# Performance work log

Measured on AMD Instinct MI355X. Metric: run time of the kernel, lower is better.

Reference implementation:

```python
import jax, jax.numpy as jnp
import numpy as np
import math

B, N, D, H, K = 8, 256, 128, 256, 128


def setup_inputs() -> dict:
    key = jax.random.key(0)
    ks = jax.random.split(key, 8)
    # forward args
    x = jax.random.uniform(ks[0], (B, N, N), dtype=jnp.float32) * 3.0  # pairwise distances
    atom_embeds = jax.random.normal(ks[1], (B, N, D), dtype=jnp.float32)
    # params of nn.Linear(2D, H) and nn.Linear(H, 2) (store as [in, out])
    lim1 = 1.0 / math.sqrt(2 * D)
    W1 = jax.random.uniform(ks[2], (2 * D, H), minval=-lim1, maxval=lim1, dtype=jnp.float32)
    b1 = jax.random.uniform(ks[3], (H,), minval=-lim1, maxval=lim1, dtype=jnp.float32)
    lim2 = 1.0 / math.sqrt(H)
    W2 = jax.random.uniform(ks[4], (H, 2), minval=-lim2, maxval=lim2, dtype=jnp.float32)
    b2 = jax.random.uniform(ks[5], (2,), minval=-lim2, maxval=lim2, dtype=jnp.float32)
    # RBF params: means ~ U(0,3), temps ~ U(0.1,10)
    means = jax.random.uniform(ks[6], (K,), minval=0.0, maxval=3.0, dtype=jnp.float32)
    temps = jax.random.uniform(ks[7], (K,), minval=0.1, maxval=10.0, dtype=jnp.float32)
    return {"x": x, "atom_embeds": atom_embeds, "W1": W1, "b1": b1,
            "W2": W2, "b2": b2, "means": means, "temps": temps}


def reference(x, atom_embeds, W1, b1, W2, b2, means, temps):
    d = atom_embeds.shape[-1]
    scale = 1.0 / math.sqrt(2 * d)
    # Split-weight trick: cat([e_i, e_j]) @ W1 == e_i @ W1[:D] + e_j @ W1[D:]
    # (same math, avoids materializing the [B,N,N,2D] concat)
    hi = jnp.einsum('bnd,dh->bnh', atom_embeds, W1[:d])   # [B,N,H]
    hj = jnp.einsum('bnd,dh->bnh', atom_embeds, W1[d:])   # [B,N,H]
    h = jax.nn.relu(hi[:, :, None, :] + hj[:, None, :, :] + b1)  # [B,N,N,H]
    edge_features = (jnp.einsum('bijh,ho->bijo', h, W2) + b2) * scale  # [B,N,N,2]
    mul = edge_features[..., 0:1]   # [B,N,N,1]
    bias = edge_features[..., 1:2]  # [B,N,N,1]
    v = mul * x[..., None] + bias   # [B,N,N,1]
    temp = jnp.abs(temps)
    # RBF gaussian basis expansion -> [B,N,N,K]
    return jnp.exp(-jnp.square(v - means) * temp)
```

## Files before the change

kernel.cpp:

```cpp
#include <hip/hip_runtime.h>
#include <hip/hip_bf16.h>


#define NB 8
#define NN 256
#define ND 128
#define NH 256
#define NK 128

__global__ __launch_bounds__(256) void precompute_hij(
    const float* __restrict__ atom, const float* __restrict__ W1,
    const float* __restrict__ b1,
    float* __restrict__ hi, float* __restrict__ hjbT) {
  const int h = threadIdx.x;
  const int base = blockIdx.x * 8;
  const int b  = base >> 8;
  const int j0 = base & 255;
  __shared__ float a[8][ND];
  for (int t = threadIdx.x; t < 8 * ND; t += 256) {
    a[t >> 7][t & 127] = atom[(size_t)base * ND + t];
  }
  __syncthreads();
  float acc0[8], acc1[8];
  const float bv = b1[h];
#pragma unroll
  for (int r = 0; r < 8; ++r) { acc0[r] = 0.f; acc1[r] = bv; }
  for (int d = 0; d < ND; ++d) {
    const float w0 = W1[d * NH + h];
    const float w1 = W1[(ND + d) * NH + h];
#pragma unroll
    for (int r = 0; r < 8; ++r) {
      acc0[r] = fmaf(a[r][d], w0, acc0[r]);
      acc1[r] = fmaf(a[r][d], w1, acc1[r]);
    }
  }
#pragma unroll
  for (int r = 0; r < 8; ++r) {
    hi[(size_t)(base + r) * NH + h] = acc0[r];
    hjbT[((size_t)b * NH + h) * NN + (j0 + r)] = acc1[r];
  }
}

__global__ __launch_bounds__(256) void edge_rbf(
    const float* __restrict__ x,
    const float* __restrict__ hi, const float* __restrict__ hjbT,
    const float* __restrict__ W2, const float* __restrict__ b2,
    const float* __restrict__ means, const float* __restrict__ temps,
    float* __restrict__ out) {
  const int b    = blockIdx.x & 7;
  const int i    = blockIdx.x >> 3;
  const int bi   = b * NN + i;
  const int lane = threadIdx.x & 63;
  const int wave = threadIdx.x >> 6;

  __shared__ float part0[4][NN];
  __shared__ float part1[4][NN];
  __shared__ float vsh[NN];

  const float* __restrict__ hjrow = hjbT + ((size_t)b * NH + wave * 64) * NN;
  const float* __restrict__ hirow = hi + (size_t)bi * NH + wave * 64;
  const float* __restrict__ w2row = W2 + wave * 128;

  float acc0[4] = {0.f, 0.f, 0.f, 0.f};
  float acc1[4] = {0.f, 0.f, 0.f, 0.f};
#pragma unroll 8
  for (int hh = 0; hh < 64; ++hh) {
    const float4 hj4 = *reinterpret_cast<const float4*>(hjrow + (size_t)hh * NN + 4 * lane);
    const float hih = hirow[hh];
    const float w0  = w2row[2 * hh];
    const float w1  = w2row[2 * hh + 1];
    float a0 = fmaxf(hih + hj4.x, 0.f);
    float a1 = fmaxf(hih + hj4.y, 0.f);
    float a2 = fmaxf(hih + hj4.z, 0.f);
    float a3 = fmaxf(hih + hj4.w, 0.f);
    acc0[0] = fmaf(a0, w0, acc0[0]); acc1[0] = fmaf(a0, w1, acc1[0]);
    acc0[1] = fmaf(a1, w0, acc0[1]); acc1[1] = fmaf(a1, w1, acc1[1]);
    acc0[2] = fmaf(a2, w0, acc0[2]); acc1[2] = fmaf(a2, w1, acc1[2]);
    acc0[3] = fmaf(a3, w0, acc0[3]); acc1[3] = fmaf(a3, w1, acc1[3]);
  }
  *reinterpret_cast<float4*>(&part0[wave][4 * lane]) = make_float4(acc0[0], acc0[1], acc0[2], acc0[3]);
  *reinterpret_cast<float4*>(&part1[wave][4 * lane]) = make_float4(acc1[0], acc1[1], acc1[2], acc1[3]);
  __syncthreads();

  {
    const int t = threadIdx.x;
    const float s0 = part0[0][t] + part0[1][t] + part0[2][t] + part0[3][t];
    const float s1 = part1[0][t] + part1[1][t] + part1[2][t] + part1[3][t];
    const float scale = 0.0625f;
    const float mul  = (s0 + b2[0]) * scale;
    const float bias = (s1 + b2[1]) * scale;
    vsh[t] = fmaf(mul, x[(size_t)bi * NN + t], bias);
  }
  __syncthreads();

  const int k0 = (lane & 31) * 4;
  const float LOG2E = 1.44269504088896340736f;
  const float4 mv = *reinterpret_cast<const float4*>(means + k0);
  float4 tv = *reinterpret_cast<const float4*>(temps + k0);
  tv.x = -fabsf(tv.x) * LOG2E;
  tv.y = -fabsf(tv.y) * LOG2E;
  tv.z = -fabsf(tv.z) * LOG2E;
  tv.w = -fabsf(tv.w) * LOG2E;

  float* __restrict__ orow = out + ((size_t)bi * NN + wave * 64) * NK;
  const int jhalf = lane >> 5;
#pragma unroll 4
  for (int c = 0; c < 32; ++c) {
    const int j = 2 * c + jhalf;
    const float vj = vsh[wave * 64 + j];
    const float d0 = vj - mv.x;
    const float d1 = vj - mv.y;
    const float d2 = vj - mv.z;
    const float d3 = vj - mv.w;
    float4 e;
    e.x = __builtin_amdgcn_exp2f(d0 * d0 * tv.x);
    e.y = __builtin_amdgcn_exp2f(d1 * d1 * tv.y);
    e.z = __builtin_amdgcn_exp2f(d2 * d2 * tv.z);
    e.w = __builtin_amdgcn_exp2f(d3 * d3 * tv.w);
    *reinterpret_cast<float4*>(orow + (size_t)j * NK + k0) = e;
  }
}

extern "C" void kernel_launch(void* const* d_in, const int* in_sizes, int n_in,
                              void* d_out, int out_size, void* d_ws, size_t ws_size,
                              hipStream_t stream) {
  const float* x     = (const float*)d_in[0];
  const float* atom  = (const float*)d_in[1];
  const float* W1    = (const float*)d_in[2];
  const float* b1    = (const float*)d_in[3];
  const float* W2    = (const float*)d_in[4];
  const float* b2    = (const float*)d_in[5];
  const float* means = (const float*)d_in[6];
  const float* temps = (const float*)d_in[7];
  float* out = (float*)d_out;

  float* hi   = (float*)d_ws;
  float* hjbT = hi + (size_t)NB * NN * NH;

  precompute_hij<<<NB * NN / 8, 256, 0, stream>>>(atom, W1, b1, hi, hjbT);
  edge_rbf<<<NB * NN, 256, 0, stream>>>(x, hi, hjbT, W2, b2, means, temps, out);
}
```

Measured before the change: 80.06 us.

## Process four i rows per block to reuse hj loads, use nontemporal output stores

Each edge_rbf block now handles GI=4 consecutive i rows, so every float4 of hjbT loaded from global memory is reused across four rows of accumulators. This cuts hjbT traffic fourfold and launches a quarter as many blocks. The output writes also switch to nontemporal stores so the large RBF tensor streams past the cache. The trade-offs are more registers per thread, more shared memory per block, and fewer blocks in flight, which could lower occupancy.

```diff
diff --git a/kernel.cpp b/kernel.cpp
--- a/kernel.cpp
+++ b/kernel.cpp
@@ -7,6 +7,9 @@
 #define ND 128
 #define NH 256
 #define NK 128
+#define GI 4
+
+typedef float f32x4 __attribute__((ext_vector_type(4)));
 
 __global__ __launch_bounds__(256) void precompute_hij(
     const float* __restrict__ atom, const float* __restrict__ W1,
@@ -48,52 +51,68 @@
     const float* __restrict__ means, const float* __restrict__ temps,
     float* __restrict__ out) {
   const int b    = blockIdx.x & 7;
-  const int i    = blockIdx.x >> 3;
-  const int bi   = b * NN + i;
+  const int i0   = (blockIdx.x >> 3) * GI;
   const int lane = threadIdx.x & 63;
   const int wave = threadIdx.x >> 6;
 
-  __shared__ float part0[4][NN];
-  __shared__ float part1[4][NN];
-  __shared__ float vsh[NN];
+  __shared__ float part0[4][GI][NN];
+  __shared__ float part1[4][GI][NN];
+  __shared__ float vsh[GI][NN];
 
-  const float* __restrict__ hjrow = hjbT + ((size_t)b * NH + wave * 64) * NN;
-  const float* __restrict__ hirow = hi + (size_t)bi * NH + wave * 64;
-  const float* __restrict__ w2row = W2 + wave * 128;
+  const float* __restrict__ hjrow  = hjbT + ((size_t)b * NH + wave * 64) * NN;
+  const float* __restrict__ w2row  = W2 + wave * 128;
+  const float* __restrict__ hibase = hi + ((size_t)(b * NN + i0)) * NH + wave * 64;
 
-  float acc0[4] = {0.f, 0.f, 0.f, 0.f};
-  float acc1[4] = {0.f, 0.f, 0.f, 0.f};
-#pragma unroll 8
+  float acc0[GI][4], acc1[GI][4];
+#pragma unroll
+  for (int r = 0; r < GI; ++r)
+#pragma unroll
+    for (int q = 0; q < 4; ++q) { acc0[r][q] = 0.f; acc1[r][q] = 0.f; }
+
+#pragma unroll 4
   for (int hh = 0; hh < 64; ++hh) {
     const float4 hj4 = *reinterpret_cast<const float4*>(hjrow + (size_t)hh * NN + 4 * lane);
-    const float hih = hirow[hh];
-    const float w0  = w2row[2 * hh];
-    const float w1  = w2row[2 * hh + 1];
-    float a0 = fmaxf(hih + hj4.x, 0.f);
-    float a1 = fmaxf(hih + hj4.y, 0.f);
-    float a2 = fmaxf(hih + hj4.z, 0.f);
-    float a3 = fmaxf(hih + hj4.w, 0.f);
-    acc0[0] = fmaf(a0, w0, acc0[0]); acc1[0] = fmaf(a0, w1, acc1[0]);
-    acc0[1] = fmaf(a1, w0, acc0[1]); acc1[1] = fmaf(a1, w1, acc1[1]);
-    acc0[2] = fmaf(a2, w0, acc0[2]); acc1[2] = fmaf(a2, w1, acc1[2]);
-    acc0[3] = fmaf(a3, w0, acc0[3]); acc1[3] = fmaf(a3, w1, acc1[3]);
+    const float w0 = w2row[2 * hh];
+    const float w1 = w2row[2 * hh + 1];
+#pragma unroll
+    for (int r = 0; r < GI; ++r) {
+      const float hih = hibase[(size_t)r * NH + hh];
+      const float a0 = fmaxf(hih + hj4.x, 0.f);
+      const float a1 = fmaxf(hih + hj4.y, 0.f);
+      const float a2 = fmaxf(hih + hj4.z, 0.f);
+      const float a3 = fmaxf(hih + hj4.w, 0.f);
+      acc0[r][0] = fmaf(a0, w0, acc0[r][0]); acc1[r][0] = fmaf(a0, w1, acc1[r][0]);
+      acc0[r][1] = fmaf(a1, w0, acc0[r][1]); acc1[r][1] = fmaf(a1, w1, acc1[r][1]);
+      acc0[r][2] = fmaf(a2, w0, acc0[r][2]); acc1[r][2] = fmaf(a2, w1, acc1[r][2]);
+      acc0[r][3] = fmaf(a3, w0, acc0[r][3]); acc1[r][3] = fmaf(a3, w1, acc1[r][3]);
+    }
   }
-  *reinterpret_cast<float4*>(&part0[wave][4 * lane]) = make_float4(acc0[0], acc0[1], acc0[2], acc0[3]);
-  *reinterpret_cast<float4*>(&part1[wave][4 * lane]) = make_float4(acc1[0], acc1[1], acc1[2], acc1[3]);
+#pragma unroll
+  for (int r = 0; r < GI; ++r) {
+    *reinterpret_cast<float4*>(&part0[wave][r][4 * lane]) =
+        make_float4(acc0[r][0], acc0[r][1], acc0[r][2], acc0[r][3]);
+    *reinterpret_cast<float4*>(&part1[wave][r][4 * lane]) =
+        make_float4(acc1[r][0], acc1[r][1], acc1[r][2], acc1[r][3]);
+  }
   __syncthreads();
 
   {
     const int t = threadIdx.x;
-    const float s0 = part0[0][t] + part0[1][t] + part0[2][t] + part0[3][t];
-    const float s1 = part1[0][t] + part1[1][t] + part1[2][t] + part1[3][t];
     const float scale = 0.0625f;
-    const float mul  = (s0 + b2[0]) * scale;
-    const float bias = (s1 + b2[1]) * scale;
-    vsh[t] = fmaf(mul, x[(size_t)bi * NN + t], bias);
+    const float b20 = b2[0], b21 = b2[1];
+#pragma unroll
+    for (int r = 0; r < GI; ++r) {
+      const float s0 = part0[0][r][t] + part0[1][r][t] + part0[2][r][t] + part0[3][r][t];
+      const float s1 = part1[0][r][t] + part1[1][r][t] + part1[2][r][t] + part1[3][r][t];
+      const float mul  = (s0 + b20) * scale;
+      const float bias = (s1 + b21) * scale;
+      vsh[r][t] = fmaf(mul, x[(size_t)(b * NN + i0 + r) * NN + t], bias);
+    }
   }
   __syncthreads();
 
   const int k0 = (lane & 31) * 4;
+  const int jhalf = lane >> 5;
   const float LOG2E = 1.44269504088896340736f;
   const float4 mv = *reinterpret_cast<const float4*>(means + k0);
   float4 tv = *reinterpret_cast<const float4*>(temps + k0);
@@ -102,22 +121,24 @@
   tv.z = -fabsf(tv.z) * LOG2E;
   tv.w = -fabsf(tv.w) * LOG2E;
 
-  float* __restrict__ orow = out + ((size_t)bi * NN + wave * 64) * NK;
-  const int jhalf = lane >> 5;
+#pragma unroll
+  for (int r = 0; r < GI; ++r) {
+    float* __restrict__ orow = out + ((size_t)(b * NN + i0 + r) * NN + wave * 64) * NK;
 #pragma unroll 4
-  for (int c = 0; c < 32; ++c) {
-    const int j = 2 * c + jhalf;
-    const float vj = vsh[wave * 64 + j];
-    const float d0 = vj - mv.x;
-    const float d1 = vj - mv.y;
-    const float d2 = vj - mv.z;
-    const float d3 = vj - mv.w;
-    float4 e;
-    e.x = __builtin_amdgcn_exp2f(d0 * d0 * tv.x);
-    e.y = __builtin_amdgcn_exp2f(d1 * d1 * tv.y);
-    e.z = __builtin_amdgcn_exp2f(d2 * d2 * tv.z);
-    e.w = __builtin_amdgcn_exp2f(d3 * d3 * tv.w);
-    *reinterpret_cast<float4*>(orow + (size_t)j * NK + k0) = e;
+    for (int c = 0; c < 32; ++c) {
+      const int j = 2 * c + jhalf;
+      const float vj = vsh[r][wave * 64 + j];
+      const float d0 = vj - mv.x;
+      const float d1 = vj - mv.y;
+      const float d2 = vj - mv.z;
+      const float d3 = vj - mv.w;
+      f32x4 e;
+      e.x = __builtin_amdgcn_exp2f(d0 * d0 * tv.x);
+      e.y = __builtin_amdgcn_exp2f(d1 * d1 * tv.y);
+      e.z = __builtin_amdgcn_exp2f(d2 * d2 * tv.z);
+      e.w = __builtin_amdgcn_exp2f(d3 * d3 * tv.w);
+      __builtin_nontemporal_store(e, reinterpret_cast<f32x4*>(orow + (size_t)j * NK + k0));
+    }
   }
 }
 
@@ -138,5 +159,5 @@
   float* hjbT = hi + (size_t)NB * NN * NH;
 
   precompute_hij<<<NB * NN / 8, 256, 0, stream>>>(atom, W1, b1, hi, hjbT);
-  edge_rbf<<<NB * NN, 256, 0, stream>>>(x, hi, hjbT, W2, b2, means, temps, out);
+  edge_rbf<<<NB * NN / GI, 256, 0, stream>>>(x, hi, hjbT, W2, b2, means, temps, out);
 }
```

New measurement: 87.96 us. 1.1x slower.
